# Kernel tuning notes

Measured on AMD Instinct MI355X. Metric: run time of the kernel, lower is better.

The kernel has to match this reference:

```python
import jax, jax.numpy as jnp
import numpy as np

N_TOKEN = 16384
N_EMBED = 512


def setup_inputs() -> dict:
    key = jax.random.key(0)
    k1, k2, k3, k4 = jax.random.split(key, 4)
    inputs = jax.random.normal(k1, (8, 2048, N_EMBED), dtype=jnp.float32)
    # nn.Linear(n_embed, n_token): weight [n_token, n_embed], bias [n_token]
    lin_w = jax.random.normal(k2, (N_TOKEN, N_EMBED), dtype=jnp.float32) * (1.0 / np.sqrt(N_EMBED))
    lin_b = jax.random.normal(k3, (N_TOKEN,), dtype=jnp.float32) * 0.01
    # nn.Embedding(n_token, n_embed) weight = value embeddings
    value_w = jax.random.normal(k4, (N_TOKEN, N_EMBED), dtype=jnp.float32)
    return {"inputs": inputs, "lin_w": lin_w, "lin_b": lin_b, "value_w": value_w}


def reference(inputs, lin_w, lin_b, value_w):
    size = inputs.shape
    x = inputs.reshape(-1, N_EMBED)                       # [T, E]
    logits = jnp.einsum('te,ne->tn', x, lin_w) + lin_b    # [T, N]
    probs = jax.nn.softmax(logits, axis=-1)               # [T, N]
    quantized = jnp.einsum('tn,ne->te', probs, value_w) + x
    return quantized.reshape(size)
```

## Files before the change

### kernel.cpp

```cpp
#include <hip/hip_runtime.h>
#include <hip/hip_bf16.h>
#include <stdint.h>

#define N_TOKEN 16384
#define N_EMBED 512
#define QBLK 64
#define KVB 32
#define NT (N_TOKEN / KVB)

typedef __attribute__((ext_vector_type(8))) short bf16x8;
typedef __attribute__((ext_vector_type(4))) short bf16x4;
typedef __attribute__((ext_vector_type(4))) float f32x4;

__device__ __forceinline__ unsigned short f2bf(float f) {
  unsigned u = __float_as_uint(f);
  u = (u + 0x7FFFu + ((u >> 16) & 1u)) >> 16;
  return (unsigned short)u;
}
__device__ __forceinline__ float bf2f(unsigned short h) {
  return __uint_as_float(((unsigned)h) << 16);
}

__device__ __forceinline__ void load_lds16(const void* g, void* l) {
  __builtin_amdgcn_global_load_lds((const __attribute__((address_space(1))) void*)g,
                                   (__attribute__((address_space(3))) void*)l, 16, 0, 0);
}

__global__ void cvt_bf16_kernel(const float* __restrict__ in, unsigned short* __restrict__ out, int n8) {
  int i = blockIdx.x * blockDim.x + threadIdx.x;
  if (i >= n8) return;
  float4 a = ((const float4*)in)[i * 2 + 0];
  float4 b = ((const float4*)in)[i * 2 + 1];
  uint4 o;
  o.x = (unsigned)f2bf(a.x) | ((unsigned)f2bf(a.y) << 16);
  o.y = (unsigned)f2bf(a.z) | ((unsigned)f2bf(a.w) << 16);
  o.z = (unsigned)f2bf(b.x) | ((unsigned)f2bf(b.y) << 16);
  o.w = (unsigned)f2bf(b.z) | ((unsigned)f2bf(b.w) << 16);
  ((uint4*)out)[i] = o;
}

__global__ void transpose_cvt_kernel(const float* __restrict__ in, unsigned short* __restrict__ out) {
  __shared__ float tile[64][65];
  int n0 = blockIdx.x * 64;
  int e0 = blockIdx.y * 64;
  int c = threadIdx.x & 63;
  int r0 = threadIdx.x >> 6;
#pragma unroll
  for (int r = r0; r < 64; r += 4)
    tile[r][c] = in[(size_t)(n0 + r) * N_EMBED + e0 + c];
  __syncthreads();
#pragma unroll
  for (int r = r0; r < 64; r += 4)
    out[(size_t)(e0 + r) * N_TOKEN + n0 + c] = f2bf(tile[c][r]);
}

__global__ __launch_bounds__(512, 1) void flash4_kernel(
    const unsigned short* __restrict__ xb,
    const unsigned short* __restrict__ kb,
    const unsigned short* __restrict__ vt,
    const float* __restrict__ bias,
    const float* __restrict__ xf,
    float* __restrict__ out)
{
  __shared__ __align__(16) unsigned char lds[65536 + 36864 + 8192 + 256];
  unsigned char* Ks = lds;
  unsigned char* Sp = lds + 65536;
  unsigned char* Pb = lds + 65536 + 36864;
  float* lsumB = (float*)(lds + 65536 + 36864 + 8192);

  const int tid = threadIdx.x;
  const int w = tid >> 6;
  const int lane = tid & 63;
  const int g = lane >> 4;
  const int l15 = lane & 15;
  const int we = w >> 1, wn = w & 1;
  const int qbase = blockIdx.x * QBLK;

  bf16x8 q[4][4];
#pragma unroll
  for (int rf = 0; rf < 4; ++rf)
#pragma unroll
    for (int kk = 0; kk < 4; ++kk)
      q[rf][kk] = *(const bf16x8*)(xb + (size_t)(qbase + 16 * rf + l15) * N_EMBED +
                                   128 * we + 32 * kk + 8 * g);

  const f32x4 fzero = {0.f, 0.f, 0.f, 0.f};
  f32x4 acc[4][4];
#pragma unroll
  for (int rf = 0; rf < 4; ++rf)
#pragma unroll
    for (int cf = 0; cf < 4; ++cf) acc[rf][cf] = fzero;
  float lsum_reg = 0.f;

  const int eq = 8 * w + (lane >> 3);
  const int ec = lane & 7;

  auto stage = [&](int half, int t) {
    const unsigned char* kg = (const unsigned char*)(kb + (size_t)t * KVB * N_EMBED);
    unsigned char* Kd = Ks + half * 32768;
#pragma unroll
    for (int it = 0; it < 4; ++it) {
      int c = tid + 512 * it;
      int row = c >> 6;
      int cb = (c & 63) * 16;
      load_lds16(kg + row * 1024 + (cb ^ ((row & 7) << 4)), Kd + c * 16);
    }
  };

  stage(0, 0);

  for (int t = 0; t < NT + 2; ++t) {
    asm volatile("s_waitcnt vmcnt(0) lgkmcnt(0)" ::: "memory");
    __builtin_amdgcn_sched_barrier(0);
    __builtin_amdgcn_s_barrier();

    bf16x8 bv[4];
    if (t >= 2) {
      const unsigned short* vbase = vt + (size_t)(t - 2) * KVB + 8 * g;
#pragma unroll
      for (int cf = 0; cf < 4; ++cf)
        bv[cf] = *(const bf16x8*)(vbase + (size_t)(64 * w + 16 * cf + l15) * N_TOKEN);
    }
    if (t + 1 < NT) stage((t + 1) & 1, t + 1);

    if (t < NT) {
      const unsigned char* Kb = Ks + (t & 1) * 32768;
      f32x4 s[4];
#pragma unroll
      for (int rf = 0; rf < 4; ++rf) s[rf] = fzero;
      const int krow = 16 * wn + l15;
      __builtin_amdgcn_s_setprio(1);
#pragma unroll
      for (int kk = 0; kk < 4; ++kk) {
        int cb = 256 * we + 64 * kk + 16 * g;
        bf16x8 bk = *(const bf16x8*)(Kb + krow * 1024 + (cb ^ ((krow & 7) << 4)));
#pragma unroll
        for (int rf = 0; rf < 4; ++rf)
          s[rf] = __builtin_amdgcn_mfma_f32_16x16x32_bf16(q[rf][kk], bk, s[rf], 0, 0, 0);
      }
      __builtin_amdgcn_s_setprio(0);
      unsigned char* sp = Sp + (t & 1) * 18432 + we * 4608;
#pragma unroll
      for (int rf = 0; rf < 4; ++rf)
#pragma unroll
        for (int j = 0; j < 4; ++j) {
          int qq = 16 * rf + 4 * g + j;
          *(unsigned short*)(sp + qq * 72 + (16 * wn + l15) * 2) = f2bf(s[rf][j]);
        }
    }

    if (t >= 1 && t <= NT) {
      const unsigned char* sp = Sp + ((t - 1) & 1) * 18432;
      int off = eq * 72 + ec * 8;
      bf16x4 p0 = *(const bf16x4*)(sp + off);
      bf16x4 p1 = *(const bf16x4*)(sp + 4608 + off);
      bf16x4 p2 = *(const bf16x4*)(sp + 9216 + off);
      bf16x4 p3 = *(const bf16x4*)(sp + 13824 + off);
      float4 bb = *(const float4*)(bias + (t - 1) * KVB + 4 * ec);
      float l0 = bf2f((unsigned short)p0[0]) + bf2f((unsigned short)p1[0]) +
                 bf2f((unsigned short)p2[0]) + bf2f((unsigned short)p3[0]) + bb.x;
      float l1 = bf2f((unsigned short)p0[1]) + bf2f((unsigned short)p1[1]) +
                 bf2f((unsigned short)p2[1]) + bf2f((unsigned short)p3[1]) + bb.y;
      float l2 = bf2f((unsigned short)p0[2]) + bf2f((unsigned short)p1[2]) +
                 bf2f((unsigned short)p2[2]) + bf2f((unsigned short)p3[2]) + bb.z;
      float l3 = bf2f((unsigned short)p0[3]) + bf2f((unsigned short)p1[3]) +
                 bf2f((unsigned short)p2[3]) + bf2f((unsigned short)p3[3]) + bb.w;
      float e0 = exp2f(l0 * 1.44269504f);
      float e1 = exp2f(l1 * 1.44269504f);
      float e2 = exp2f(l2 * 1.44269504f);
      float e3 = exp2f(l3 * 1.44269504f);
      lsum_reg += (e0 + e1) + (e2 + e3);
      bf16x4 pw;
      pw[0] = (short)f2bf(e0);
      pw[1] = (short)f2bf(e1);
      pw[2] = (short)f2bf(e2);
      pw[3] = (short)f2bf(e3);
      *(bf16x4*)(Pb + ((t - 1) & 1) * 4096 + eq * 64 + ec * 8) = pw;
    }

    if (t >= 2) {
      const unsigned char* pb = Pb + (t & 1) * 4096;
      bf16x8 pa[4];
#pragma unroll
      for (int rf = 0; rf < 4; ++rf)
        pa[rf] = *(const bf16x8*)(pb + (16 * rf + l15) * 64 + g * 16);
      __builtin_amdgcn_s_setprio(1);
#pragma unroll
      for (int cf = 0; cf < 4; ++cf)
#pragma unroll
        for (int rf = 0; rf < 4; ++rf)
          acc[rf][cf] = __builtin_amdgcn_mfma_f32_16x16x32_bf16(pa[rf], bv[cf], acc[rf][cf], 0, 0, 0);
      __builtin_amdgcn_s_setprio(0);
    }
  }

  {
    float r = lsum_reg;
    r += __shfl_xor(r, 1, 64);
    r += __shfl_xor(r, 2, 64);
    r += __shfl_xor(r, 4, 64);
    if (ec == 0) lsumB[eq] = r;
  }
  __syncthreads();
#pragma unroll
  for (int rf = 0; rf < 4; ++rf)
#pragma unroll
    for (int j = 0; j < 4; ++j) {
      int qq = 16 * rf + 4 * g + j;
      float inv = 1.0f / lsumB[qq];
      int row = qbase + qq;
#pragma unroll
      for (int cf = 0; cf < 4; ++cf) {
        int col = 64 * w + 16 * cf + l15;
        size_t idx = (size_t)row * N_EMBED + col;
        out[idx] = acc[rf][cf][j] * inv + xf[idx];
      }
    }
}

extern "C" void kernel_launch(void* const* d_in, const int* in_sizes, int n_in,
                              void* d_out, int out_size, void* d_ws, size_t ws_size,
                              hipStream_t stream) {
  const float* x = (const float*)d_in[0];
  const float* lin_w = (const float*)d_in[1];
  const float* lin_b = (const float*)d_in[2];
  const float* value_w = (const float*)d_in[3];
  float* outp = (float*)d_out;

  unsigned short* xb = (unsigned short*)d_ws;
  unsigned short* wb = (unsigned short*)((char*)d_ws + (16 << 20));
  unsigned short* vt = (unsigned short*)((char*)d_ws + (32 << 20));

  const int n8 = (N_TOKEN * N_EMBED) / 8;
  cvt_bf16_kernel<<<n8 / 256, 256, 0, stream>>>(x, xb, n8);
  cvt_bf16_kernel<<<n8 / 256, 256, 0, stream>>>(lin_w, wb, n8);
  transpose_cvt_kernel<<<dim3(N_TOKEN / 64, N_EMBED / 64), 256, 0, stream>>>(value_w, vt);
  flash4_kernel<<<N_TOKEN / QBLK, 512, 0, stream>>>(xb, wb, vt, lin_b, x, outp);
}
```

Before: 1.076 ms.

## Halve query block to 32 rows and remap waves for more blocks

The query tile per block drops from 64 to 32 rows, doubling the grid to 512 blocks, and the wave roles are remapped so each wave handles one 16-row query slice across two embedding halves. The QK MFMA operands are swapped so S comes out transposed, and pairs are packed into 32-bit LDS stores with hardware bf16x2 conversion. This reduces the cross-wave logit reduction from four partials to two and cuts the LDS scratch size. The aim is better CU occupancy and less LDS traffic, at the cost of re-streaming the K and V matrices from L2 twice as many times.

New measurement: 2.069 ms. 92.3% more time.

```diff
diff --git a/kernel.cpp b/kernel.cpp
--- a/kernel.cpp
+++ b/kernel.cpp
@@ -4,12 +4,11 @@
 
 #define N_TOKEN 16384
 #define N_EMBED 512
-#define QBLK 64
+#define QBLK 32
 #define KVB 32
 #define NT (N_TOKEN / KVB)
 
 typedef __attribute__((ext_vector_type(8))) short bf16x8;
-typedef __attribute__((ext_vector_type(4))) short bf16x4;
 typedef __attribute__((ext_vector_type(4))) float f32x4;
 
 __device__ __forceinline__ unsigned short f2bf(float f) {
@@ -17,8 +16,20 @@
   u = (u + 0x7FFFu + ((u >> 16) & 1u)) >> 16;
   return (unsigned short)u;
 }
-__device__ __forceinline__ float bf2f(unsigned short h) {
-  return __uint_as_float(((unsigned)h) << 16);
+__device__ __forceinline__ float bfhi2f(unsigned u) {
+  return __uint_as_float(u & 0xFFFF0000u);
+}
+__device__ __forceinline__ float bflo2f(unsigned u) {
+  return __uint_as_float(u << 16);
+}
+__device__ __forceinline__ unsigned pk2(float a, float b) {
+  float2 f;
+  f.x = a;
+  f.y = b;
+  __hip_bfloat162 h = __float22bfloat162_rn(f);
+  unsigned u;
+  __builtin_memcpy(&u, &h, 4);
+  return u;
 }
 
 __device__ __forceinline__ void load_lds16(const void* g, void* l) {
@@ -54,7 +65,7 @@
     out[(size_t)(e0 + r) * N_TOKEN + n0 + c] = f2bf(tile[c][r]);
 }
 
-__global__ __launch_bounds__(512, 1) void flash4_kernel(
+__global__ __launch_bounds__(512, 4) void flash5_kernel(
     const unsigned short* __restrict__ xb,
     const unsigned short* __restrict__ kb,
     const unsigned short* __restrict__ vt,
@@ -62,38 +73,42 @@
     const float* __restrict__ xf,
     float* __restrict__ out)
 {
-  __shared__ __align__(16) unsigned char lds[65536 + 36864 + 8192 + 256];
+  __shared__ __align__(16) unsigned char lds[65536 + 9216 + 5120 + 128];
   unsigned char* Ks = lds;
   unsigned char* Sp = lds + 65536;
-  unsigned char* Pb = lds + 65536 + 36864;
-  float* lsumB = (float*)(lds + 65536 + 36864 + 8192);
+  unsigned char* Pb = lds + 65536 + 9216;
+  float* lsumB = (float*)(lds + 65536 + 9216 + 5120);
 
   const int tid = threadIdx.x;
   const int w = tid >> 6;
   const int lane = tid & 63;
   const int g = lane >> 4;
   const int l15 = lane & 15;
-  const int we = w >> 1, wn = w & 1;
+  const int we = w & 1, wn = (w >> 1) & 1, wq = w >> 2;
   const int qbase = blockIdx.x * QBLK;
 
-  bf16x8 q[4][4];
-#pragma unroll
-  for (int rf = 0; rf < 4; ++rf)
-#pragma unroll
-    for (int kk = 0; kk < 4; ++kk)
-      q[rf][kk] = *(const bf16x8*)(xb + (size_t)(qbase + 16 * rf + l15) * N_EMBED +
-                                   128 * we + 32 * kk + 8 * g);
+  const int eq = tid >> 4;
+  const int ekp = tid & 15;
+
+  bf16x8 q[8];
+#pragma unroll
+  for (int kk = 0; kk < 8; ++kk)
+    q[kk] = *(const bf16x8*)(xb + (size_t)(qbase + 16 * wq + l15) * N_EMBED + 256 * we + 32 * kk + 8 * g);
 
   const f32x4 fzero = {0.f, 0.f, 0.f, 0.f};
-  f32x4 acc[4][4];
-#pragma unroll
-  for (int rf = 0; rf < 4; ++rf)
+  f32x4 acc[2][4];
+#pragma unroll
+  for (int rf = 0; rf < 2; ++rf)
 #pragma unroll
     for (int cf = 0; cf < 4; ++cf) acc[rf][cf] = fzero;
   float lsum_reg = 0.f;
 
-  const int eq = 8 * w + (lane >> 3);
-  const int ec = lane & 7;
+  const int spw_off = we * 2304 + (16 * wq + l15) * 72 + 32 * wn + 8 * g;
+  const int spr_off = eq * 72 + ekp * 4;
+  const int pbw_off = eq * 80 + ekp * 4;
+  const int pbr0 = l15 * 80 + 16 * g;
+  const int pbr1 = (16 + l15) * 80 + 16 * g;
+  const int krow = 16 * wn + l15;
 
   auto stage = [&](int half, int t) {
     const unsigned char* kg = (const unsigned char*)(kb + (size_t)t * KVB * N_EMBED);
@@ -114,82 +129,65 @@
     __builtin_amdgcn_sched_barrier(0);
     __builtin_amdgcn_s_barrier();
 
+    unsigned su0 = 0, su1 = 0;
+    if (t >= 1 && t <= NT) {
+      const unsigned char* sp = Sp + ((t - 1) & 1) * 4608 + spr_off;
+      su0 = *(const unsigned*)(sp);
+      su1 = *(const unsigned*)(sp + 2304);
+    }
+    bf16x8 pb0 = {}, pb1 = {};
     bf16x8 bv[4];
     if (t >= 2) {
-      const unsigned short* vbase = vt + (size_t)(t - 2) * KVB + 8 * g;
+      const unsigned char* pb = Pb + (t & 1) * 2560;
+      pb0 = *(const bf16x8*)(pb + pbr0);
+      pb1 = *(const bf16x8*)(pb + pbr1);
+      const unsigned short* vbase = vt + (size_t)(64 * w + l15) * N_TOKEN + (t - 2) * KVB + 8 * g;
 #pragma unroll
       for (int cf = 0; cf < 4; ++cf)
-        bv[cf] = *(const bf16x8*)(vbase + (size_t)(64 * w + 16 * cf + l15) * N_TOKEN);
-    }
+        bv[cf] = *(const bf16x8*)(vbase + (size_t)(16 * cf) * N_TOKEN);
+    }
+    float2 bb = {0.f, 0.f};
+    if (t >= 1 && t <= NT) bb = *(const float2*)(bias + (t - 1) * KVB + 2 * ekp);
+
     if (t + 1 < NT) stage((t + 1) & 1, t + 1);
 
     if (t < NT) {
-      const unsigned char* Kb = Ks + (t & 1) * 32768;
-      f32x4 s[4];
-#pragma unroll
-      for (int rf = 0; rf < 4; ++rf) s[rf] = fzero;
-      const int krow = 16 * wn + l15;
+      const unsigned char* Kb = Ks + (t & 1) * 32768 + krow * 1024;
+      f32x4 c0 = fzero, c1 = fzero;
       __builtin_amdgcn_s_setprio(1);
 #pragma unroll
       for (int kk = 0; kk < 4; ++kk) {
-        int cb = 256 * we + 64 * kk + 16 * g;
-        bf16x8 bk = *(const bf16x8*)(Kb + krow * 1024 + (cb ^ ((krow & 7) << 4)));
-#pragma unroll
-        for (int rf = 0; rf < 4; ++rf)
-          s[rf] = __builtin_amdgcn_mfma_f32_16x16x32_bf16(q[rf][kk], bk, s[rf], 0, 0, 0);
+        int cb0 = 512 * we + 64 * kk + 16 * g;
+        int cb1 = cb0 + 256;
+        bf16x8 bk0 = *(const bf16x8*)(Kb + (cb0 ^ ((krow & 7) << 4)));
+        bf16x8 bk1 = *(const bf16x8*)(Kb + (cb1 ^ ((krow & 7) << 4)));
+        c0 = __builtin_amdgcn_mfma_f32_16x16x32_bf16(bk0, q[kk], c0, 0, 0, 0);
+        c1 = __builtin_amdgcn_mfma_f32_16x16x32_bf16(bk1, q[kk + 4], c1, 0, 0, 0);
       }
       __builtin_amdgcn_s_setprio(0);
-      unsigned char* sp = Sp + (t & 1) * 18432 + we * 4608;
-#pragma unroll
-      for (int rf = 0; rf < 4; ++rf)
-#pragma unroll
-        for (int j = 0; j < 4; ++j) {
-          int qq = 16 * rf + 4 * g + j;
-          *(unsigned short*)(sp + qq * 72 + (16 * wn + l15) * 2) = f2bf(s[rf][j]);
-        }
+      f32x4 c = c0 + c1;
+      uint2 wv;
+      wv.x = pk2(c[0], c[1]);
+      wv.y = pk2(c[2], c[3]);
+      *(uint2*)(Sp + (t & 1) * 4608 + spw_off) = wv;
     }
 
     if (t >= 1 && t <= NT) {
-      const unsigned char* sp = Sp + ((t - 1) & 1) * 18432;
-      int off = eq * 72 + ec * 8;
-      bf16x4 p0 = *(const bf16x4*)(sp + off);
-      bf16x4 p1 = *(const bf16x4*)(sp + 4608 + off);
-      bf16x4 p2 = *(const bf16x4*)(sp + 9216 + off);
-      bf16x4 p3 = *(const bf16x4*)(sp + 13824 + off);
-      float4 bb = *(const float4*)(bias + (t - 1) * KVB + 4 * ec);
-      float l0 = bf2f((unsigned short)p0[0]) + bf2f((unsigned short)p1[0]) +
-                 bf2f((unsigned short)p2[0]) + bf2f((unsigned short)p3[0]) + bb.x;
-      float l1 = bf2f((unsigned short)p0[1]) + bf2f((unsigned short)p1[1]) +
-                 bf2f((unsigned short)p2[1]) + bf2f((unsigned short)p3[1]) + bb.y;
-      float l2 = bf2f((unsigned short)p0[2]) + bf2f((unsigned short)p1[2]) +
-                 bf2f((unsigned short)p2[2]) + bf2f((unsigned short)p3[2]) + bb.z;
-      float l3 = bf2f((unsigned short)p0[3]) + bf2f((unsigned short)p1[3]) +
-                 bf2f((unsigned short)p2[3]) + bf2f((unsigned short)p3[3]) + bb.w;
-      float e0 = exp2f(l0 * 1.44269504f);
-      float e1 = exp2f(l1 * 1.44269504f);
-      float e2 = exp2f(l2 * 1.44269504f);
-      float e3 = exp2f(l3 * 1.44269504f);
-      lsum_reg += (e0 + e1) + (e2 + e3);
-      bf16x4 pw;
-      pw[0] = (short)f2bf(e0);
-      pw[1] = (short)f2bf(e1);
-      pw[2] = (short)f2bf(e2);
-      pw[3] = (short)f2bf(e3);
-      *(bf16x4*)(Pb + ((t - 1) & 1) * 4096 + eq * 64 + ec * 8) = pw;
+      float lo = bflo2f(su0) + bflo2f(su1) + bb.x;
+      float hi = bfhi2f(su0) + bfhi2f(su1) + bb.y;
+      float e0 = exp2f(lo * 1.44269504f);
+      float e1 = exp2f(hi * 1.44269504f);
+      lsum_reg += e0 + e1;
+      *(unsigned*)(Pb + ((t - 1) & 1) * 2560 + pbw_off) = pk2(e0, e1);
     }
 
     if (t >= 2) {
-      const unsigned char* pb = Pb + (t & 1) * 4096;
-      bf16x8 pa[4];
-#pragma unroll
-      for (int rf = 0; rf < 4; ++rf)
-        pa[rf] = *(const bf16x8*)(pb + (16 * rf + l15) * 64 + g * 16);
       __builtin_amdgcn_s_setprio(1);
 #pragma unroll
-      for (int cf = 0; cf < 4; ++cf)
-#pragma unroll
-        for (int rf = 0; rf < 4; ++rf)
-          acc[rf][cf] = __builtin_amdgcn_mfma_f32_16x16x32_bf16(pa[rf], bv[cf], acc[rf][cf], 0, 0, 0);
+      for (int cf = 0; cf < 4; ++cf) {
+        acc[0][cf] = __builtin_amdgcn_mfma_f32_16x16x32_bf16(bv[cf], pb0, acc[0][cf], 0, 0, 0);
+        acc[1][cf] = __builtin_amdgcn_mfma_f32_16x16x32_bf16(bv[cf], pb1, acc[1][cf], 0, 0, 0);
+      }
       __builtin_amdgcn_s_setprio(0);
     }
   }
@@ -199,23 +197,24 @@
     r += __shfl_xor(r, 1, 64);
     r += __shfl_xor(r, 2, 64);
     r += __shfl_xor(r, 4, 64);
-    if (ec == 0) lsumB[eq] = r;
+    r += __shfl_xor(r, 8, 64);
+    if (ekp == 0) lsumB[eq] = r;
   }
   __syncthreads();
-#pragma unroll
-  for (int rf = 0; rf < 4; ++rf)
-#pragma unroll
-    for (int j = 0; j < 4; ++j) {
-      int qq = 16 * rf + 4 * g + j;
-      float inv = 1.0f / lsumB[qq];
-      int row = qbase + qq;
-#pragma unroll
-      for (int cf = 0; cf < 4; ++cf) {
-        int col = 64 * w + 16 * cf + l15;
+
+#pragma unroll
+  for (int rf = 0; rf < 2; ++rf) {
+    float inv = 1.0f / lsumB[16 * rf + l15];
+    int row = qbase + 16 * rf + l15;
+#pragma unroll
+    for (int cf = 0; cf < 4; ++cf)
+#pragma unroll
+      for (int j = 0; j < 4; ++j) {
+        int col = 64 * w + 16 * cf + 4 * g + j;
         size_t idx = (size_t)row * N_EMBED + col;
         out[idx] = acc[rf][cf][j] * inv + xf[idx];
       }
-    }
+  }
 }
 
 extern "C" void kernel_launch(void* const* d_in, const int* in_sizes, int n_in,
@@ -235,5 +234,5 @@
   cvt_bf16_kernel<<<n8 / 256, 256, 0, stream>>>(x, xb, n8);
   cvt_bf16_kernel<<<n8 / 256, 256, 0, stream>>>(lin_w, wb, n8);
   transpose_cvt_kernel<<<dim3(N_TOKEN / 64, N_EMBED / 64), 256, 0, stream>>>(value_w, vt);
-  flash4_kernel<<<N_TOKEN / QBLK, 512, 0, stream>>>(xb, wb, vt, lin_b, x, outp);
-}
+  flash5_kernel<<<N_TOKEN / QBLK, 512, 0, stream>>>(xb, wb, vt, lin_b, x, outp);
+}
```
